# Performance work log

Measured on AMD Instinct MI355X. Metric: run time of the kernel, lower is better.

## Reference

```python
import jax, jax.numpy as jnp
import numpy as np

EMBED = 1024
HEADS = 16
HEAD_DIM = EMBED // HEADS
B, S = 4, 2048


def setup_inputs() -> dict:
    key = jax.random.key(0)
    ks = jax.random.split(key, 8)
    values = jax.random.normal(ks[0], (B, S, EMBED), dtype=jnp.float32)
    keys_in = jax.random.normal(ks[1], (B, S, EMBED), dtype=jnp.float32)
    query = jax.random.normal(ks[2], (B, S, EMBED), dtype=jnp.float32)
    mask = jnp.ones((B, 1, 1, S), dtype=jnp.int32)
    sc = 1.0 / np.sqrt(HEAD_DIM)
    Wv = jax.random.normal(ks[3], (HEAD_DIM, HEAD_DIM), dtype=jnp.float32) * sc
    Wk = jax.random.normal(ks[4], (HEAD_DIM, HEAD_DIM), dtype=jnp.float32) * sc
    Wq = jax.random.normal(ks[5], (HEAD_DIM, HEAD_DIM), dtype=jnp.float32) * sc
    Wo = jax.random.normal(ks[6], (EMBED, EMBED), dtype=jnp.float32) * (1.0 / np.sqrt(EMBED))
    bo = jnp.zeros((EMBED,), dtype=jnp.float32)
    return {"values": values, "keys": keys_in, "query": query, "mask": mask,
            "Wv": Wv, "Wk": Wk, "Wq": Wq, "Wo": Wo, "bo": bo}


def reference(values, keys, query, mask, Wv, Wk, Wq, Wo, bo):
    n = query.shape[0]
    vl, kl, ql = values.shape[1], keys.shape[1], query.shape[1]
    h, d = HEADS, HEAD_DIM
    # split heads: [n, len, h, d]
    v = values.reshape(n, vl, h, d)
    k = keys.reshape(n, kl, h, d)
    q = query.reshape(n, ql, h, d)
    # per-head linear projections (torch Linear: x @ W.T), shared across heads
    v = jnp.einsum('nlhd,ed->nlhe', v, Wv)
    k = jnp.einsum('nlhd,ed->nlhe', k, Wk)
    q = jnp.einsum('nlhd,ed->nlhe', q, Wq)
    # attention scores [n, h, q, k]
    energy = jnp.einsum('nqhd,nkhd->nhqk', q, k)
    energy = jnp.where(mask == 0, jnp.float32(-1e20), energy)
    # NOTE: original scales by sqrt(embed_size), not sqrt(head_dim)
    attn = jax.nn.softmax(energy / jnp.sqrt(jnp.float32(EMBED)), axis=3)
    out = jnp.einsum('nhql,nlhd->nqhd', attn, v).reshape(n, ql, h * d)
    return out @ Wo.T + bo
```

## Files before the change

### kernel.cpp

```cpp
#include <hip/hip_runtime.h>
#include <hip/hip_bf16.h>


#define SS 2048
#define HH 16
#define DD 64

typedef __attribute__((ext_vector_type(8))) short bf16x8;
typedef __attribute__((ext_vector_type(4))) short s16x4;
typedef __attribute__((ext_vector_type(4))) float f32x4;
typedef __attribute__((ext_vector_type(16))) float f32x16;

__device__ __forceinline__ short f2bf(float f) {
  union { float f; unsigned u; } c; c.f = f;
  unsigned r = (c.u + 0x7FFFu + ((c.u >> 16) & 1u)) >> 16;
  return (short)r;
}

__device__ __forceinline__ int cvtpk(float lo, float hi) {
  int r;
  asm("v_cvt_pk_bf16_f32 %0, %1, %2" : "=v"(r) : "v"(lo), "v"(hi));
  return r;
}

__device__ __forceinline__ float fexp2(float x) {
  float r;
  asm("v_exp_f32 %0, %1" : "=v"(r) : "v"(x));
  return r;
}

__global__ __launch_bounds__(256) void proj_kernel(
    const float* __restrict__ xq, const float* __restrict__ xk, const float* __restrict__ xv,
    const float* __restrict__ Wq, const float* __restrict__ Wk, const float* __restrict__ Wv,
    short* __restrict__ qp, short* __restrict__ kp, short* __restrict__ vp)
{
  __shared__ short xlds[128][72];
  __shared__ short wlds[3][64][72];
  const int t = threadIdx.x;
  const int lane = t & 63;
  const int w = t >> 6;
  const int l15 = lane & 15, l4 = lane >> 4;

  const float* wsrc[3] = {Wq, Wk, Wv};
#pragma unroll
  for (int z = 0; z < 3; ++z) {
#pragma unroll
    for (int i = 0; i < 4; ++i) {
      int fi = (t + i * 256) * 4;
      int row = fi >> 6, col = fi & 63;
      float4 a = *(const float4*)(wsrc[z] + fi);
      s16x4 sv = { f2bf(a.x), f2bf(a.y), f2bf(a.z), f2bf(a.w) };
      *(s16x4*)&wlds[z][row][col] = sv;
    }
  }

  const long r0 = (long)blockIdx.x * 128;
  const float* xin[3] = {xq, xk, xv};
  short* outp[3] = {qp, kp, vp};
  const float SCQ = 0.03125f * 1.4426950408889634f;

#pragma unroll
  for (int z = 0; z < 3; ++z) {
    __syncthreads();
    const float* src = xin[z] + r0 * 64;
#pragma unroll
    for (int i = 0; i < 8; ++i) {
      int fi = (t + i * 256) * 4;
      int row = fi >> 6, col = fi & 63;
      float4 a = *(const float4*)(src + fi);
      s16x4 sv = { f2bf(a.x), f2bf(a.y), f2bf(a.z), f2bf(a.w) };
      *(s16x4*)&xlds[row][col] = sv;
    }
    __syncthreads();

    bf16x8 af[2][2];
#pragma unroll
    for (int mi = 0; mi < 2; ++mi)
#pragma unroll
      for (int kb = 0; kb < 2; ++kb)
        af[mi][kb] = *(const bf16x8*)&xlds[w * 32 + mi * 16 + l15][kb * 32 + l4 * 8];

    f32x4 acc[2][4];
#pragma unroll
    for (int mi = 0; mi < 2; ++mi)
#pragma unroll
      for (int nt = 0; nt < 4; ++nt)
        acc[mi][nt] = (f32x4){0.f, 0.f, 0.f, 0.f};

#pragma unroll
    for (int nt = 0; nt < 4; ++nt)
#pragma unroll
      for (int kb = 0; kb < 2; ++kb) {
        bf16x8 bfr = *(const bf16x8*)&wlds[z][nt * 16 + l15][kb * 32 + l4 * 8];
#pragma unroll
        for (int mi = 0; mi < 2; ++mi)
          acc[mi][nt] = __builtin_amdgcn_mfma_f32_16x16x32_bf16(af[mi][kb], bfr, acc[mi][nt], 0, 0, 0);
      }

    short* dst = outp[z];
    const float sc = (z == 0) ? SCQ : 1.0f;
#pragma unroll
    for (int mi = 0; mi < 2; ++mi)
#pragma unroll
      for (int nt = 0; nt < 4; ++nt)
#pragma unroll
        for (int j = 0; j < 4; ++j) {
          int r = (int)r0 + w * 32 + mi * 16 + l4 * 4 + j;
          int e = nt * 16 + l15;
          int h = r & 15, bs = r >> 4;
          int b = bs >> 11, s = bs & 2047;
          dst[(((long)(b * 16 + h) * 2048 + s) << 6) + e] = f2bf(acc[mi][nt][j] * sc);
        }
  }
}

__global__ __launch_bounds__(256) void wo_cvt(const float* __restrict__ Wo,
                                              short* __restrict__ wob) {
  long i = ((long)blockIdx.x * 256 + threadIdx.x) * 4;
  float4 a = *(const float4*)(Wo + i);
  s16x4 sv = { f2bf(a.x), f2bf(a.y), f2bf(a.z), f2bf(a.w) };
  *(s16x4*)(wob + i) = sv;
}

__global__ __launch_bounds__(256) void vt_kernel(const short* __restrict__ vp,
                                                 short* __restrict__ vpt) {
  __shared__ short tl[64][72];
  const int t = threadIdx.x;
  const long base_in = (long)blockIdx.y * SS * DD + (long)blockIdx.x * 64 * DD;
#pragma unroll
  for (int i = 0; i < 2; ++i) {
    int c = t + i * 256;
    int s = c >> 3, d0 = (c & 7) * 8;
    bf16x8 v = *(const bf16x8*)(vp + base_in + s * 64 + d0);
#pragma unroll
    for (int j = 0; j < 8; ++j) tl[d0 + j][s] = v[j];
  }
  __syncthreads();
  const long base_out = (long)blockIdx.y * DD * SS + (long)blockIdx.x * 64;
#pragma unroll
  for (int i = 0; i < 2; ++i) {
    int c = t + i * 256;
    int d = c >> 3, s0 = (c & 7) * 8;
    *(bf16x8*)(vpt + base_out + (long)d * SS + s0) = *(const bf16x8*)&tl[d][s0];
  }
}

__global__ __launch_bounds__(256, 4) void attn_kernel(
    const short* __restrict__ qp, const short* __restrict__ kp, const short* __restrict__ vpt,
    const int* __restrict__ mask, short* __restrict__ ao)
{
  __shared__ short klds[2][64][72];
  __shared__ short vtlds[2][64][72];
  __shared__ int tile_ok[32];
  const int t = threadIdx.x, lane = t & 63, w = t >> 6;
  const int l31 = lane & 31, hi = lane >> 5;
  const int wg = (blockIdx.x & 7) * 128 + (blockIdx.x >> 3);
  const int bh = wg >> 4, qt = wg & 15;
  const int b = bh >> 4, h = bh & 15;
  const short* qb  = qp + (long)bh * SS * DD;
  const short* kbp = kp + (long)bh * SS * DD;
  const short* vtp = vpt + (long)bh * DD * SS;
  const int* mb = mask + b * SS;

  if (t < 32) tile_ok[t] = 1;
  __syncthreads();
  {
    int ok = 1;
#pragma unroll
    for (int i = 0; i < 8; ++i) ok &= (mb[t * 8 + i] != 0);
    if (!ok) tile_ok[t >> 3] = 0;
  }

  const int q = qt * 128 + w * 32 + l31;
  bf16x8 qf[4];
#pragma unroll
  for (int dblk = 0; dblk < 4; ++dblk)
    qf[dblk] = *(const bf16x8*)(qb + (long)q * 64 + dblk * 16 + hi * 8);

  const int sr = t >> 2;
  const int sc = (t & 3) * 16;
  const int v5 = sr & 31;
  const int prow = (sr & 32) + (v5 & 3) + 4 * ((v5 >> 3) & 1)
                 + 8 * (2 * ((v5 >> 4) & 1) + ((v5 >> 2) & 1));
  const short* kr_ptr = kbp + (long)sr * 64 + sc;
  const short* vr_ptr = vtp + (long)sr * SS + sc;

  bf16x8 kr0 = *(const bf16x8*)(kr_ptr);
  bf16x8 kr1 = *(const bf16x8*)(kr_ptr + 8);
  bf16x8 vr0 = *(const bf16x8*)(vr_ptr);
  bf16x8 vr1 = *(const bf16x8*)(vr_ptr + 8);
  *(bf16x8*)&klds[0][prow][sc]      = kr0;
  *(bf16x8*)&klds[0][prow][sc + 8]  = kr1;
  *(bf16x8*)&vtlds[0][sr][sc]       = vr0;
  *(bf16x8*)&vtlds[0][sr][sc + 8]   = vr1;
  kr0 = *(const bf16x8*)(kr_ptr + 64 * 64);
  kr1 = *(const bf16x8*)(kr_ptr + 64 * 64 + 8);
  vr0 = *(const bf16x8*)(vr_ptr + 64);
  vr1 = *(const bf16x8*)(vr_ptr + 64 + 8);

  const f32x16 fzero = {0.f,0.f,0.f,0.f,0.f,0.f,0.f,0.f,
                        0.f,0.f,0.f,0.f,0.f,0.f,0.f,0.f};
  f32x16 oacc[2];
  oacc[0] = fzero; oacc[1] = fzero;
  float l_reg = 0.f;

  for (int kt = 0; kt < SS / 64; ++kt) {
    const int cur = kt & 1, nxt = cur ^ 1;
    const int k0 = kt * 64;
    __syncthreads();
    *(bf16x8*)&klds[nxt][prow][sc]      = kr0;
    *(bf16x8*)&klds[nxt][prow][sc + 8]  = kr1;
    *(bf16x8*)&vtlds[nxt][sr][sc]       = vr0;
    *(bf16x8*)&vtlds[nxt][sr][sc + 8]   = vr1;

    f32x16 sacc[2];
    __builtin_amdgcn_s_setprio(1);
#pragma unroll
    for (int kb = 0; kb < 2; ++kb) {
      bf16x8 ka0 = *(const bf16x8*)&klds[cur][kb * 32 + l31][hi * 8];
      sacc[kb] = __builtin_amdgcn_mfma_f32_32x32x16_bf16(ka0, qf[0], fzero, 0, 0, 0);
#pragma unroll
      for (int dblk = 1; dblk < 4; ++dblk) {
        bf16x8 ka = *(const bf16x8*)&klds[cur][kb * 32 + l31][dblk * 16 + hi * 8];
        sacc[kb] = __builtin_amdgcn_mfma_f32_32x32x16_bf16(ka, qf[dblk], sacc[kb], 0, 0, 0);
      }
    }
    __builtin_amdgcn_s_setprio(0);

    if (!tile_ok[kt]) {
#pragma unroll
      for (int kb = 0; kb < 2; ++kb)
#pragma unroll
        for (int r = 0; r < 16; ++r) {
          int kv = k0 + kb * 32 + 16 * ((r >> 3) & 1) + 8 * hi
                 + 4 * ((r >> 2) & 1) + (r & 3);
          if (mb[kv] == 0) sacc[kb][r] = -1e30f;
        }
    }

    float s0 = 0.f, s1 = 0.f, s2 = 0.f, s3 = 0.f;
#pragma unroll
    for (int kb = 0; kb < 2; ++kb)
#pragma unroll
      for (int r = 0; r < 16; r += 4) {
        float p0 = fexp2(sacc[kb][r]);
        float p1 = fexp2(sacc[kb][r + 1]);
        float p2 = fexp2(sacc[kb][r + 2]);
        float p3 = fexp2(sacc[kb][r + 3]);
        sacc[kb][r] = p0; sacc[kb][r + 1] = p1;
        sacc[kb][r + 2] = p2; sacc[kb][r + 3] = p3;
        s0 += p0; s1 += p1; s2 += p2; s3 += p3;
      }
    float sum = (s0 + s1) + (s2 + s3);
    sum += __shfl_xor(sum, 32);
    l_reg += sum;

    union PW { int wd[4]; bf16x8 v; } pa[4];
#pragma unroll
    for (int kb = 0; kb < 2; ++kb)
#pragma unroll
      for (int s1i = 0; s1i < 2; ++s1i)
#pragma unroll
        for (int w2 = 0; w2 < 4; ++w2)
          pa[kb * 2 + s1i].wd[w2] =
              cvtpk(sacc[kb][8 * s1i + 2 * w2], sacc[kb][8 * s1i + 2 * w2 + 1]);

    __builtin_amdgcn_s_setprio(1);
#pragma unroll
    for (int dt = 0; dt < 2; ++dt)
#pragma unroll
      for (int ks = 0; ks < 4; ++ks) {
        bf16x8 va = *(const bf16x8*)&vtlds[cur][dt * 32 + l31][ks * 16 + hi * 8];
        oacc[dt] = __builtin_amdgcn_mfma_f32_32x32x16_bf16(va, pa[ks].v, oacc[dt], 0, 0, 0);
      }
    __builtin_amdgcn_s_setprio(0);

    {
      const int ktn = (kt < 30) ? kt + 2 : 31;
      const long k0n = (long)ktn * 64;
      kr0 = *(const bf16x8*)(kr_ptr + k0n * 64);
      kr1 = *(const bf16x8*)(kr_ptr + k0n * 64 + 8);
      vr0 = *(const bf16x8*)(vr_ptr + k0n);
      vr1 = *(const bf16x8*)(vr_ptr + k0n + 8);
    }
  }

  float inv = 1.f / l_reg;
#pragma unroll
  for (int dt = 0; dt < 2; ++dt)
#pragma unroll
    for (int g = 0; g < 4; ++g) {
      s16x4 sv;
#pragma unroll
      for (int j = 0; j < 4; ++j) sv[j] = f2bf(oacc[dt][g * 4 + j] * inv);
      int d0 = dt * 32 + g * 8 + hi * 4;
      *(s16x4*)(ao + (long)(b * SS + q) * 1024 + h * 64 + d0) = sv;
    }
}

__global__ __launch_bounds__(256) void out_gemm(
    const short* __restrict__ ao, const short* __restrict__ wob,
    const float* __restrict__ bo, float* __restrict__ out)
{
  __shared__ short alds[2][128][72];
  __shared__ short blds[2][128][72];
  const int t = threadIdx.x, lane = t & 63, w = t >> 6;
  const int l15 = lane & 15, l4 = lane >> 4;
  const int wm = w >> 1, wn = w & 1;
  const long m0 = (long)blockIdx.y * 128;
  const int n0 = blockIdx.x * 128;

  const int srow = t >> 3;
  const int scol = (t & 7) * 8;

  f32x4 acc[4][4];
#pragma unroll
  for (int mi = 0; mi < 4; ++mi)
#pragma unroll
    for (int ni = 0; ni < 4; ++ni) acc[mi][ni] = (f32x4){0.f, 0.f, 0.f, 0.f};

  bf16x8 ar[4], br[4];
#pragma unroll
  for (int i = 0; i < 4; ++i) {
    int row = srow + i * 32;
    ar[i] = *(const bf16x8*)(ao + (m0 + row) * 1024 + scol);
    br[i] = *(const bf16x8*)(wob + (long)(n0 + row) * 1024 + scol);
  }
#pragma unroll
  for (int i = 0; i < 4; ++i) {
    int row = srow + i * 32;
    *(bf16x8*)&alds[0][row][scol] = ar[i];
    *(bf16x8*)&blds[0][row][scol] = br[i];
  }
#pragma unroll
  for (int i = 0; i < 4; ++i) {
    int row = srow + i * 32;
    ar[i] = *(const bf16x8*)(ao + (m0 + row) * 1024 + 64 + scol);
    br[i] = *(const bf16x8*)(wob + (long)(n0 + row) * 1024 + 64 + scol);
  }

  for (int ki = 0; ki < 16; ++ki) {
    const int cur = ki & 1, nxt = cur ^ 1;
    __syncthreads();
#pragma unroll
    for (int i = 0; i < 4; ++i) {
      int row = srow + i * 32;
      *(bf16x8*)&alds[nxt][row][scol] = ar[i];
      *(bf16x8*)&blds[nxt][row][scol] = br[i];
    }
#pragma unroll
    for (int kb = 0; kb < 2; ++kb) {
      bf16x8 af[4], bfr[4];
#pragma unroll
      for (int mi = 0; mi < 4; ++mi)
        af[mi] = *(const bf16x8*)&alds[cur][wm * 64 + mi * 16 + l15][kb * 32 + l4 * 8];
#pragma unroll
      for (int ni = 0; ni < 4; ++ni)
        bfr[ni] = *(const bf16x8*)&blds[cur][wn * 64 + ni * 16 + l15][kb * 32 + l4 * 8];
#pragma unroll
      for (int mi = 0; mi < 4; ++mi)
#pragma unroll
        for (int ni = 0; ni < 4; ++ni)
          acc[mi][ni] = __builtin_amdgcn_mfma_f32_16x16x32_bf16(af[mi], bfr[ni], acc[mi][ni], 0, 0, 0);
    }
    {
      const int kn = ((ki < 14) ? ki + 2 : 15) * 64;
#pragma unroll
      for (int i = 0; i < 4; ++i) {
        int row = srow + i * 32;
        ar[i] = *(const bf16x8*)(ao + (m0 + row) * 1024 + kn + scol);
        br[i] = *(const bf16x8*)(wob + (long)(n0 + row) * 1024 + kn + scol);
      }
    }
  }
#pragma unroll
  for (int ni = 0; ni < 4; ++ni) {
    float bias = bo[n0 + wn * 64 + ni * 16 + l15];
#pragma unroll
    for (int mi = 0; mi < 4; ++mi)
#pragma unroll
      for (int j = 0; j < 4; ++j)
        out[(m0 + wm * 64 + mi * 16 + l4 * 4 + j) * 1024 + n0 + wn * 64 + ni * 16 + l15] =
            acc[mi][ni][j] + bias;
  }
}

extern "C" void kernel_launch(void* const* d_in, const int* in_sizes, int n_in,
                              void* d_out, int out_size, void* d_ws, size_t ws_size,
                              hipStream_t stream) {
  const float* values = (const float*)d_in[0];
  const float* keys   = (const float*)d_in[1];
  const float* query  = (const float*)d_in[2];
  const int*   mask   = (const int*)d_in[3];
  const float* Wv     = (const float*)d_in[4];
  const float* Wk     = (const float*)d_in[5];
  const float* Wq     = (const float*)d_in[6];
  const float* Wo     = (const float*)d_in[7];
  const float* bo     = (const float*)d_in[8];
  float* out = (float*)d_out;

  const long NTOK = 4L * SS * HH * DD;
  short* qp  = (short*)d_ws;
  short* kp  = qp + NTOK;
  short* vp  = kp + NTOK;
  short* aot = vp + NTOK;
  short* wob = aot + NTOK;
  short* vpt = wob + 1024 * 1024;

  hipLaunchKernelGGL(proj_kernel, dim3(1024), dim3(256), 0, stream,
                     query, keys, values, Wq, Wk, Wv, qp, kp, vp);
  hipLaunchKernelGGL(wo_cvt, dim3(1024), dim3(256), 0, stream, Wo, wob);
  hipLaunchKernelGGL(vt_kernel, dim3(32, 64), dim3(256), 0, stream, vp, vpt);
  hipLaunchKernelGGL(attn_kernel, dim3(1024), dim3(256), 0, stream,
                     qp, kp, vpt, mask, aot);
  hipLaunchKernelGGL(out_gemm, dim3(8, 64), dim3(256), 0, stream,
                     aot, wob, bo, out);
}
```

Baseline: 143.2 us.

## Split attention KV range across two wave groups and combine partials via LDS

The attention block grows from 256 to 512 threads. Two groups of four waves each process half of the key/value sequence for the same 128 queries, and the partial output accumulators and row sums are merged through shared memory at the end. The next-tile global prefetch is also issued right after the QK MFMAs instead of at the end of the iteration. This doubles the waves available per query tile to hide latency, at the cost of more LDS, a combine step, and possible occupancy pressure from the larger block. The LDS row padding is reduced from 72 to 68 shorts, which may change bank conflicts.

```diff
diff --git a/kernel.cpp b/kernel.cpp
--- a/kernel.cpp
+++ b/kernel.cpp
@@ -10,6 +10,8 @@
 typedef __attribute__((ext_vector_type(4))) short s16x4;
 typedef __attribute__((ext_vector_type(4))) float f32x4;
 typedef __attribute__((ext_vector_type(16))) float f32x16;
+
+#define MFMA32(A, B, C) __builtin_amdgcn_mfma_f32_32x32x16_bf16((A), (B), (C), 0, 0, 0)
 
 __device__ __forceinline__ short f2bf(float f) {
   union { float f; unsigned u; } c; c.f = f;
@@ -145,15 +147,18 @@
   }
 }
 
-__global__ __launch_bounds__(256, 4) void attn_kernel(
+#define KL(G, D) smem[0][G][D]
+#define VL(G, D) smem[1][G][D]
+
+__global__ __launch_bounds__(512, 4) void attn_kernel(
     const short* __restrict__ qp, const short* __restrict__ kp, const short* __restrict__ vpt,
     const int* __restrict__ mask, short* __restrict__ ao)
 {
-  __shared__ short klds[2][64][72];
-  __shared__ short vtlds[2][64][72];
+  __shared__ short smem[2][2][2][64][68];
   __shared__ int tile_ok[32];
   const int t = threadIdx.x, lane = t & 63, w = t >> 6;
   const int l31 = lane & 31, hi = lane >> 5;
+  const int g = w >> 2, wq = w & 3;
   const int wg = (blockIdx.x & 7) * 128 + (blockIdx.x >> 3);
   const int bh = wg >> 4, qt = wg & 15;
   const int b = bh >> 4, h = bh & 15;
@@ -167,34 +172,36 @@
   {
     int ok = 1;
 #pragma unroll
-    for (int i = 0; i < 8; ++i) ok &= (mb[t * 8 + i] != 0);
-    if (!ok) tile_ok[t >> 3] = 0;
-  }
-
-  const int q = qt * 128 + w * 32 + l31;
+    for (int i = 0; i < 4; ++i) ok &= (mb[t * 4 + i] != 0);
+    if (!ok) tile_ok[t >> 4] = 0;
+  }
+
+  const int q = qt * 128 + wq * 32 + l31;
   bf16x8 qf[4];
 #pragma unroll
   for (int dblk = 0; dblk < 4; ++dblk)
     qf[dblk] = *(const bf16x8*)(qb + (long)q * 64 + dblk * 16 + hi * 8);
 
-  const int sr = t >> 2;
-  const int sc = (t & 3) * 16;
+  const int tl = t & 255;
+  const int sr = tl >> 2;
+  const int sc = (tl & 3) * 16;
   const int v5 = sr & 31;
   const int prow = (sr & 32) + (v5 & 3) + 4 * ((v5 >> 3) & 1)
                  + 8 * (2 * ((v5 >> 4) & 1) + ((v5 >> 2) & 1));
-  const short* kr_ptr = kbp + (long)sr * 64 + sc;
-  const short* vr_ptr = vtp + (long)sr * SS + sc;
+  const int tb = g * 16;
+  const short* kr_ptr = kbp + (long)tb * 4096 + (long)sr * 64 + sc;
+  const short* vr_ptr = vtp + (long)sr * SS + tb * 64 + sc;
 
   bf16x8 kr0 = *(const bf16x8*)(kr_ptr);
   bf16x8 kr1 = *(const bf16x8*)(kr_ptr + 8);
   bf16x8 vr0 = *(const bf16x8*)(vr_ptr);
   bf16x8 vr1 = *(const bf16x8*)(vr_ptr + 8);
-  *(bf16x8*)&klds[0][prow][sc]      = kr0;
-  *(bf16x8*)&klds[0][prow][sc + 8]  = kr1;
-  *(bf16x8*)&vtlds[0][sr][sc]       = vr0;
-  *(bf16x8*)&vtlds[0][sr][sc + 8]   = vr1;
-  kr0 = *(const bf16x8*)(kr_ptr + 64 * 64);
-  kr1 = *(const bf16x8*)(kr_ptr + 64 * 64 + 8);
+  *(bf16x8*)&KL(g, 0)[prow][sc]      = kr0;
+  *(bf16x8*)&KL(g, 0)[prow][sc + 8]  = kr1;
+  *(bf16x8*)&VL(g, 0)[sr][sc]        = vr0;
+  *(bf16x8*)&VL(g, 0)[sr][sc + 8]    = vr1;
+  kr0 = *(const bf16x8*)(kr_ptr + 4096);
+  kr1 = *(const bf16x8*)(kr_ptr + 4096 + 8);
   vr0 = *(const bf16x8*)(vr_ptr + 64);
   vr1 = *(const bf16x8*)(vr_ptr + 64 + 8);
 
@@ -204,28 +211,39 @@
   oacc[0] = fzero; oacc[1] = fzero;
   float l_reg = 0.f;
 
-  for (int kt = 0; kt < SS / 64; ++kt) {
-    const int cur = kt & 1, nxt = cur ^ 1;
+  union PW { int wd[4]; bf16x8 v; };
+
+  for (int i = 0; i < 16; ++i) {
+    const int cur = i & 1, nxt = cur ^ 1;
+    const int kt = tb + i;
     const int k0 = kt * 64;
     __syncthreads();
-    *(bf16x8*)&klds[nxt][prow][sc]      = kr0;
-    *(bf16x8*)&klds[nxt][prow][sc + 8]  = kr1;
-    *(bf16x8*)&vtlds[nxt][sr][sc]       = vr0;
-    *(bf16x8*)&vtlds[nxt][sr][sc + 8]   = vr1;
+    *(bf16x8*)&KL(g, nxt)[prow][sc]      = kr0;
+    *(bf16x8*)&KL(g, nxt)[prow][sc + 8]  = kr1;
+    *(bf16x8*)&VL(g, nxt)[sr][sc]        = vr0;
+    *(bf16x8*)&VL(g, nxt)[sr][sc + 8]    = vr1;
 
     f32x16 sacc[2];
     __builtin_amdgcn_s_setprio(1);
 #pragma unroll
     for (int kb = 0; kb < 2; ++kb) {
-      bf16x8 ka0 = *(const bf16x8*)&klds[cur][kb * 32 + l31][hi * 8];
-      sacc[kb] = __builtin_amdgcn_mfma_f32_32x32x16_bf16(ka0, qf[0], fzero, 0, 0, 0);
+      bf16x8 ka0 = *(const bf16x8*)&KL(g, cur)[kb * 32 + l31][hi * 8];
+      sacc[kb] = MFMA32(ka0, qf[0], fzero);
 #pragma unroll
       for (int dblk = 1; dblk < 4; ++dblk) {
-        bf16x8 ka = *(const bf16x8*)&klds[cur][kb * 32 + l31][dblk * 16 + hi * 8];
-        sacc[kb] = __builtin_amdgcn_mfma_f32_32x32x16_bf16(ka, qf[dblk], sacc[kb], 0, 0, 0);
+        bf16x8 ka = *(const bf16x8*)&KL(g, cur)[kb * 32 + l31][dblk * 16 + hi * 8];
+        sacc[kb] = MFMA32(ka, qf[dblk], sacc[kb]);
       }
     }
     __builtin_amdgcn_s_setprio(0);
+
+    {
+      const int ofn = (i < 14) ? i + 2 : 15;
+      kr0 = *(const bf16x8*)(kr_ptr + (long)ofn * 4096);
+      kr1 = *(const bf16x8*)(kr_ptr + (long)ofn * 4096 + 8);
+      vr0 = *(const bf16x8*)(vr_ptr + ofn * 64);
+      vr1 = *(const bf16x8*)(vr_ptr + ofn * 64 + 8);
+    }
 
     if (!tile_ok[kt]) {
 #pragma unroll
@@ -255,7 +273,7 @@
     sum += __shfl_xor(sum, 32);
     l_reg += sum;
 
-    union PW { int wd[4]; bf16x8 v; } pa[4];
+    PW pa[4];
 #pragma unroll
     for (int kb = 0; kb < 2; ++kb)
 #pragma unroll
@@ -270,32 +288,49 @@
     for (int dt = 0; dt < 2; ++dt)
 #pragma unroll
       for (int ks = 0; ks < 4; ++ks) {
-        bf16x8 va = *(const bf16x8*)&vtlds[cur][dt * 32 + l31][ks * 16 + hi * 8];
-        oacc[dt] = __builtin_amdgcn_mfma_f32_32x32x16_bf16(va, pa[ks].v, oacc[dt], 0, 0, 0);
+        bf16x8 va = *(const bf16x8*)&VL(g, cur)[dt * 32 + l31][ks * 16 + hi * 8];
+        oacc[dt] = MFMA32(va, pa[ks].v, oacc[dt]);
       }
     __builtin_amdgcn_s_setprio(0);
-
-    {
-      const int ktn = (kt < 30) ? kt + 2 : 31;
-      const long k0n = (long)ktn * 64;
-      kr0 = *(const bf16x8*)(kr_ptr + k0n * 64);
-      kr1 = *(const bf16x8*)(kr_ptr + k0n * 64 + 8);
-      vr0 = *(const bf16x8*)(vr_ptr + k0n);
-      vr1 = *(const bf16x8*)(vr_ptr + k0n + 8);
-    }
-  }
-
-  float inv = 1.f / l_reg;
-#pragma unroll
-  for (int dt = 0; dt < 2; ++dt)
-#pragma unroll
-    for (int g = 0; g < 4; ++g) {
-      s16x4 sv;
-#pragma unroll
-      for (int j = 0; j < 4; ++j) sv[j] = f2bf(oacc[dt][g * 4 + j] * inv);
-      int d0 = dt * 32 + g * 8 + hi * 4;
-      *(s16x4*)(ao + (long)(b * SS + q) * 1024 + h * 64 + d0) = sv;
-    }
+  }
+
+  __syncthreads();
+  float* cmb = (float*)&smem[0][0][0][0][0];
+  const int pbase = (wq * 64 + lane) * 36;
+  if (g == 1) {
+#pragma unroll
+    for (int dt = 0; dt < 2; ++dt)
+#pragma unroll
+      for (int c = 0; c < 4; ++c) {
+        f32x4 v = { oacc[dt][c * 4 + 0], oacc[dt][c * 4 + 1],
+                    oacc[dt][c * 4 + 2], oacc[dt][c * 4 + 3] };
+        *(f32x4*)&cmb[pbase + dt * 16 + c * 4] = v;
+      }
+    cmb[pbase + 32] = l_reg;
+  }
+  __syncthreads();
+  if (g == 0) {
+    l_reg += cmb[pbase + 32];
+#pragma unroll
+    for (int dt = 0; dt < 2; ++dt)
+#pragma unroll
+      for (int c = 0; c < 4; ++c) {
+        f32x4 v = *(const f32x4*)&cmb[pbase + dt * 16 + c * 4];
+#pragma unroll
+        for (int j = 0; j < 4; ++j) oacc[dt][c * 4 + j] += v[j];
+      }
+    float inv = 1.f / l_reg;
+#pragma unroll
+    for (int dt = 0; dt < 2; ++dt)
+#pragma unroll
+      for (int gg = 0; gg < 4; ++gg) {
+        s16x4 sv;
+#pragma unroll
+        for (int j = 0; j < 4; ++j) sv[j] = f2bf(oacc[dt][gg * 4 + j] * inv);
+        int d0 = dt * 32 + gg * 8 + hi * 4;
+        *(s16x4*)(ao + (long)(b * SS + q) * 1024 + h * 64 + d0) = sv;
+      }
+  }
 }
 
 __global__ __launch_bounds__(256) void out_gemm(
@@ -411,7 +446,7 @@
                      query, keys, values, Wq, Wk, Wv, qp, kp, vp);
   hipLaunchKernelGGL(wo_cvt, dim3(1024), dim3(256), 0, stream, Wo, wob);
   hipLaunchKernelGGL(vt_kernel, dim3(32, 64), dim3(256), 0, stream, vp, vpt);
-  hipLaunchKernelGGL(attn_kernel, dim3(1024), dim3(256), 0, stream,
+  hipLaunchKernelGGL(attn_kernel, dim3(1024), dim3(512), 0, stream,
                      qp, kp, vpt, mask, aot);
   hipLaunchKernelGGL(out_gemm, dim3(8, 64), dim3(256), 0, stream,
                      aot, wob, bo, out);
```

Result: slower. 157.4 us (+9.9%).
